# Kernel optimization log

Hardware: AMD Instinct MI355X
Metric: run time of the kernel (lower is better)

The kernel has to match this reference:

```python
import jax, jax.numpy as jnp
import numpy as np

N_WIN = 8
NUM_HEADS = 8
TOPK = 4
D_MODEL = 128
SCALE = D_MODEL ** (-0.5)


def setup_inputs() -> dict:
    key = jax.random.key(0)
    k1, k2 = jax.random.split(key)
    cv_feature = jax.random.normal(k1, (1, 128, 128, 128), dtype=jnp.float32)
    mv_feature = jax.random.normal(k2, (1, 2, 128, 128, 128), dtype=jnp.float32)
    return {"cv_feature": cv_feature, "mv_feature": mv_feature}


def reference(cv_feature, mv_feature):
    # cv_feature: [N, H, W, C] query view; mv_feature: [N, V, H, W, C] multi-view KV
    N, H, W, C = cv_feature.shape
    V = mv_feature.shape[1]
    j = i = N_WIN
    h, w = H // j, W // i
    p2, w2 = j * i, h * w
    ch = C // NUM_HEADS  # per-head dim

    # window partition: n (j h) (i w) c -> n (j i) h w c
    cv_patch = cv_feature.reshape(N, j, h, i, w, C).transpose(0, 1, 3, 2, 4, 5).reshape(N, p2, h, w, C)
    mv_patch = mv_feature.reshape(N, V, j, h, i, w, C).transpose(0, 1, 2, 4, 3, 5, 6).reshape(N, V, p2, h, w, C)

    q_pix = cv_patch.reshape(N, p2, w2, C)          # [N, p2, w2, C]
    kv_pix = mv_patch.reshape(N, V, p2, w2, C)      # [N, V, p2, w2, C]

    # window-level descriptors (means) -> routing logits
    q_win = cv_patch.mean(axis=(2, 3))              # [N, p2, C]
    k_win = mv_patch.mean(axis=(3, 4))              # [N, V, p2, C]

    # TopK routing (detached in original; forward math identical)
    k_flat = k_win.reshape(N, V * p2, C)
    attn_logit = jnp.einsum('npc,nqc->npq', q_win * SCALE, k_flat)  # [N, p2, V*p2]
    topk_logit, r_idx = jax.lax.top_k(attn_logit, TOPK)
    r_weight = jax.nn.softmax(topk_logit, axis=-1)  # computed by module, unused downstream

    # KV gather of selected windows: [N, p2, topk, w2, C]
    kv_flat = kv_pix.reshape(N, V * p2, w2, C)
    kv_sel = kv_flat[jnp.arange(N)[:, None, None], r_idx]

    # per-window multi-head attention over topk*w2 gathered tokens
    q = q_pix.reshape(N, p2, w2, NUM_HEADS, ch)
    kv = kv_sel.reshape(N, p2, TOPK * w2, NUM_HEADS, ch)
    attn = jnp.einsum('npwmc,npxmc->npmwx', q * SCALE, kv)  # [N, p2, m, w2, topk*w2]
    attn = jax.nn.softmax(attn, axis=-1)
    out = jnp.einsum('npmwx,npxmc->npwmc', attn, kv)        # [N, p2, w2, m, ch]

    # merge windows back: n (j i) (h w) c -> n (j h) (i w) c
    out = out.reshape(N, j, i, h, w, C).transpose(0, 1, 3, 2, 4, 5).reshape(N, H, W, C)
    return out
```

## Files before the change

### kernel.cpp

```cpp
#include <hip/hip_runtime.h>

#define HH_ 128
#define WW_ 128
#define CC_ 128
#define P2 64
#define W2 256
#define NH 8
#define CH 16
#define NV 2
#define TOPK 4
#define SCALE 0.08838834764831845f

typedef unsigned short u16;
typedef unsigned int   u32;
typedef short s8v __attribute__((ext_vector_type(8)));
typedef float f4  __attribute__((ext_vector_type(4)));

union FRAG { uint4 q; u32 u[4]; s8v v; };

__device__ float g_means[(P2 + NV * P2) * CC_];
__device__ int2  g_part[64];
__device__ int   g_mode;
__device__ int   g_amb;

__device__ inline u16 f2b(float v) {
    union { float f; u32 u; } x; x.f = v;
    u32 r = x.u + 0x7FFFu + ((x.u >> 16) & 1u);
    return (u16)(r >> 16);
}
__device__ inline float b2f(u16 h) {
    union { u32 u; float f; } x; x.u = (u32)h << 16; return x.f;
}
__device__ inline float h2f(u16 h) {
    u32 s = (h >> 15) & 1u, e = (h >> 10) & 31u, m = h & 1023u;
    float v;
    if (e == 0)       v = m * 5.9604644775e-8f;
    else if (e == 31) v = 65504.f;
    else { union { u32 u; float f; } x; x.u = ((e + 112u) << 23) | (m << 13); v = x.f; }
    return s ? -v : v;
}
__device__ inline u16 f2h(float v) {
    union { float f; u32 u; } x; x.f = v;
    u32 s = (x.u >> 16) & 0x8000u;
    int  e = (int)((x.u >> 23) & 0xFF) - 112;
    u32  m = x.u & 0x7FFFFF;
    if (e >= 31) return (u16)(s | 0x7BFF);
    if (e <= 0) {
        if (e < -10) return (u16)s;
        m |= 0x800000u;
        int sh = 14 - e;
        u32 r = m >> sh, rem = m & ((1u << sh) - 1u), half = 1u << (sh - 1);
        if (rem > half || (rem == half && (r & 1))) r++;
        return (u16)(s | r);
    }
    u32 r = ((u32)e << 10) | (m >> 13), rem = m & 0x1FFFu;
    if (rem > 0x1000u || (rem == 0x1000u && (r & 1))) r++;
    return (u16)(s | r);
}

__device__ inline u32 pkhi(float a, float b) {
    union { float f; u32 u; } xa, xb; xa.f = a; xb.f = b;
    return (xa.u >> 16) | (xb.u & 0xFFFF0000u);
}
__device__ inline float hipart(float a) {
    union { float f; u32 u; } x; x.f = a; x.u &= 0xFFFF0000u; return x.f;
}

template<int MODE>
__device__ inline float4 loadf4(const void* __restrict__ src, int off) {
    if (MODE == 0) return *(const float4*)((const float*)src + off);
    uint2 v = *(const uint2*)((const u16*)src + off);
    float4 r;
    if (MODE == 1) {
        r.x = b2f((u16)v.x); r.y = b2f((u16)(v.x >> 16));
        r.z = b2f((u16)v.y); r.w = b2f((u16)(v.y >> 16));
    } else {
        r.x = h2f((u16)v.x); r.y = h2f((u16)(v.x >> 16));
        r.z = h2f((u16)v.y); r.w = h2f((u16)(v.y >> 16));
    }
    return r;
}

template<int MODE>
__device__ inline void load16t(const void* __restrict__ src, int off, float* __restrict__ f) {
    if (MODE == 0) {
        const float4* p4 = (const float4*)((const float*)src + off);
#pragma unroll
        for (int i = 0; i < 4; ++i) {
            float4 v = p4[i];
            f[4 * i] = v.x; f[4 * i + 1] = v.y; f[4 * i + 2] = v.z; f[4 * i + 3] = v.w;
        }
    } else {
        const uint4* p4 = (const uint4*)((const u16*)src + off);
#pragma unroll
        for (int i = 0; i < 2; ++i) {
            uint4 v = p4[i];
            u32 wd[4] = { v.x, v.y, v.z, v.w };
#pragma unroll
            for (int j = 0; j < 4; ++j) {
                u16 lo = (u16)(wd[j] & 0xFFFFu), hi = (u16)(wd[j] >> 16);
                f[8 * i + 2 * j]     = (MODE == 1) ? b2f(lo) : h2f(lo);
                f[8 * i + 2 * j + 1] = (MODE == 1) ? b2f(hi) : h2f(hi);
            }
        }
    }
}

template<int MODE>
__device__ inline void store4t(void* __restrict__ out, int off, const float* __restrict__ r) {
    if (MODE == 0) {
        *(float4*)((float*)out + off) = make_float4(r[0], r[1], r[2], r[3]);
    } else if (MODE == 1) {
        u32 w0 = (u32)f2b(r[0]) | ((u32)f2b(r[1]) << 16);
        u32 w1 = (u32)f2b(r[2]) | ((u32)f2b(r[3]) << 16);
        *(uint2*)((u16*)out + off) = make_uint2(w0, w1);
    } else {
        u32 w0 = (u32)f2h(r[0]) | ((u32)f2h(r[1]) << 16);
        u32 w1 = (u32)f2h(r[2]) | ((u32)f2h(r[3]) << 16);
        *(uint2*)((u16*)out + off) = make_uint2(w0, w1);
    }
}

__global__ void detect_sample(const void* __restrict__ cv, int n) {
    __shared__ int bc[2];
    int tid = threadIdx.x, k = blockIdx.x;
    if (tid < 2) bc[tid] = 0;
    __syncthreads();
    int lim32 = n / 2;
    int lim16 = n / 2;
    u32 r = ((u32)(tid + k * 257) * 2654435761u);
    int j32 = (int)(r % (u32)lim32);
    float a = fabsf(((const float*)cv)[j32]);
    bool c0 = (a >= 1e-4f && a <= 1e4f);
    int j16 = 2 * (int)((r >> 8) % (u32)lim16);
    float b = fabsf(b2f(((const u16*)cv)[j16]));
    bool c1 = (b >= 1e-4f && b <= 1e4f);
    unsigned long long b0 = __ballot(c0);
    unsigned long long b1 = __ballot(c1);
    if ((tid & 63) == 0) {
        atomicAdd(&bc[0], __popcll(b0));
        atomicAdd(&bc[1], __popcll(b1));
    }
    __syncthreads();
    if (tid == 0) g_part[k] = make_int2(bc[0], bc[1]);
}

__global__ void detect_final() {
    int tid = threadIdx.x;
    int2 v = g_part[tid];
    int c0 = v.x, c1 = v.y;
#pragma unroll
    for (int off = 32; off >= 1; off >>= 1) {
        c0 += __shfl_down(c0, off);
        c1 += __shfl_down(c1, off);
    }
    if (tid == 0) {
        const float T = 256.f * 64.f;
        float f0 = c0 / T, f1 = c1 / T;
        int mode, amb = 0;
        if (f1 >= 0.85f) mode = 1;
        else if (f0 >= 0.80f) mode = 0;
        else mode = 2;
        if ((f1 > 0.60f && f1 < 0.85f) || (mode != 1 && f0 > 0.65f && f0 < 0.80f)) amb = 1;
        g_mode = mode; g_amb = amb;
    }
}

__global__ __launch_bounds__(512) void win_mean_kernel(const void* __restrict__ cv,
                                                       const void* __restrict__ mv) {
    __shared__ float sred[512];
    int mode = g_mode;
    int row = blockIdx.x;
    int tid = threadIdx.x;
    int c = tid & 127, q4 = tid >> 7;
    const void* src; size_t voff = 0; int p;
    if (row < P2) { p = row; src = cv; }
    else { int r = row - P2; voff = (size_t)(r >> 6) * HH_ * WW_ * CC_; p = r & 63; src = mv; }
    int jj = p >> 3, ii = p & 7;
    size_t base = voff + ((size_t)(jj * 16 + q4 * 4) * WW_ + ii * 16) * CC_ + c;
    float acc = 0.f;
    if (mode == 0) {
        const float* sp = (const float*)src;
        for (int hh = 0; hh < 4; ++hh) {
#pragma unroll
            for (int ww = 0; ww < 16; ++ww)
                acc += sp[base + ((size_t)hh * WW_ + ww) * CC_];
        }
    } else if (mode == 1) {
        const u16* sp = (const u16*)src;
        for (int hh = 0; hh < 4; ++hh) {
#pragma unroll
            for (int ww = 0; ww < 16; ++ww)
                acc += b2f(sp[base + ((size_t)hh * WW_ + ww) * CC_]);
        }
    } else {
        const u16* sp = (const u16*)src;
        for (int hh = 0; hh < 4; ++hh) {
#pragma unroll
            for (int ww = 0; ww < 16; ++ww)
                acc += h2f(sp[base + ((size_t)hh * WW_ + ww) * CC_]);
        }
    }
    sred[tid] = acc;
    __syncthreads();
    if (tid < 128) {
        float s = sred[tid] + sred[tid + 128] + sred[tid + 256] + sred[tid + 384];
        g_means[row * CC_ + tid] = s * (1.0f / 256.0f);
    }
}

template<int MODE>
__device__ void attn_body(const void* __restrict__ cv, const void* __restrict__ mv,
                          void* __restrict__ out, int p, int m, int tid,
                          u32 (* __restrict__ vfrag)[64][4], const int* __restrict__ rwin) {
    int jj = p >> 3, ii = p & 7;

#pragma unroll
    for (int it = 0; it < 2; ++it) {
        int kr = tid + it * 512;
        int kt = kr >> 4, r = kr & 15, g = r >> 2, iofs = r & 3;
        int t = rwin[kr >> 8];
        int v = t >> 6, pp = t & 63;
        int jj2 = pp >> 3, ii2 = pp & 7;
        int hh = (kr >> 4) & 15, ww = r;
        int kvbase = ((v * HH_ + jj2 * 16 + hh) * WW_ + ii2 * 16 + ww) * CC_ + m * CH;
        float f[CH];
        load16t<MODE>(mv, kvbase, f);
#pragma unroll
        for (int c = 0; c < CH; ++c) {
            union { float ff; u32 uu; } x; x.ff = f[c];
            u16 hi = (u16)(x.uu >> 16);
            union { float ff; u32 uu; } y; y.ff = f[c] - hipart(f[c]);
            u16 lo = (u16)(y.uu >> 16);
            u16* s = (u16*)&vfrag[kt][g * 16 + c][0];
            s[iofs] = hi; s[4 + iofs] = lo;
        }
    }

    int wv = tid >> 6, l = tid & 63;
    int lg = l >> 4, lr = l & 15;
    FRAG qf1[2], qf2[2];
#pragma unroll
    for (int qi = 0; qi < 2; ++qi) {
        int qrow = wv * 32 + qi * 16 + lr;
        int hh = qrow >> 4, ww = qrow & 15;
        int pix = (jj * 16 + hh) * WW_ + (ii * 16 + ww);
        float4 qv = loadf4<MODE>(cv, pix * CC_ + m * CH + 4 * lg);
        float q0 = qv.x * SCALE, q1 = qv.y * SCALE, q2 = qv.z * SCALE, q3 = qv.w * SCALE;
        u32 h01 = pkhi(q0, q1), h23 = pkhi(q2, q3);
        u32 l01 = pkhi(q0 - hipart(q0), q1 - hipart(q1));
        u32 l23 = pkhi(q2 - hipart(q2), q3 - hipart(q3));
        qf1[qi].u[0] = h01; qf1[qi].u[1] = h23; qf1[qi].u[2] = l01; qf1[qi].u[3] = l23;
        qf2[qi].u[0] = l01; qf2[qi].u[1] = l23; qf2[qi].u[2] = h01; qf2[qi].u[3] = h23;
    }

    int wb0, wb1, wb2, wb3;
#define MKWB(G, W) { int t = rwin[G]; int v = t >> 6, pp = t & 63;            \
        int jj2 = pp >> 3, ii2 = pp & 7;                                      \
        W = ((v * HH_ + jj2 * 16) * WW_ + ii2 * 16 + lr) * CC_ + m * CH + 4 * lg; }
    MKWB(0, wb0) MKWB(1, wb1) MKWB(2, wb2) MKWB(3, wb3)
#undef MKWB

    __syncthreads();

    float4 kA0 = loadf4<MODE>(mv, wb0);
    float4 kA1 = loadf4<MODE>(mv, wb0 + WW_ * CC_);
    f4 Oacc0 = {0.f, 0.f, 0.f, 0.f};
    f4 Oacc1 = {0.f, 0.f, 0.f, 0.f};
    float lp0 = 0.f, lp1 = 0.f;
    const u32* vbase = &vfrag[0][l][0];

#pragma unroll 2
    for (int kt = 0; kt < 64; ++kt) {
        float4 kc = (kt & 1) ? kA1 : kA0;
        {
            int ktn = kt + 2; ktn = (ktn > 63) ? 63 : ktn;
            int a = (ktn < 16) ? wb0 : (ktn < 32) ? wb1 : (ktn < 48) ? wb2 : wb3;
            a += (ktn & 15) * (WW_ * CC_);
            float4 nv = loadf4<MODE>(mv, a);
            if (kt & 1) kA1 = nv; else kA0 = nv;
        }
        FRAG kf;
        kf.u[0] = pkhi(kc.x, kc.y);
        kf.u[1] = pkhi(kc.z, kc.w);
        kf.u[2] = pkhi(kc.x - hipart(kc.x), kc.y - hipart(kc.y));
        kf.u[3] = pkhi(kc.z - hipart(kc.z), kc.w - hipart(kc.w));
        FRAG vf;
        vf.q = *(const uint4*)(vbase + kt * 256);

        {
            f4 sc = {0.f, 0.f, 0.f, 0.f};
            sc = __builtin_amdgcn_mfma_f32_16x16x32_bf16(kf.v, qf1[0].v, sc, 0, 0, 0);
            sc = __builtin_amdgcn_mfma_f32_16x16x32_bf16(kf.v, qf2[0].v, sc, 0, 0, 0);
            float pe0 = __expf(fminf(sc[0], 20.f));
            float pe1 = __expf(fminf(sc[1], 20.f));
            float pe2 = __expf(fminf(sc[2], 20.f));
            float pe3 = __expf(fminf(sc[3], 20.f));
            lp0 += (pe0 + pe1) + (pe2 + pe3);
            FRAG pf1, pf2;
            pf1.u[0] = pkhi(pe0, pe1);
            pf1.u[1] = pkhi(pe2, pe3);
            pf1.u[2] = pkhi(pe0 - hipart(pe0), pe1 - hipart(pe1));
            pf1.u[3] = pkhi(pe2 - hipart(pe2), pe3 - hipart(pe3));
            pf2.u[0] = pf1.u[2]; pf2.u[1] = pf1.u[3];
            pf2.u[2] = pf1.u[0]; pf2.u[3] = pf1.u[1];
            Oacc0 = __builtin_amdgcn_mfma_f32_16x16x32_bf16(vf.v, pf1.v, Oacc0, 0, 0, 0);
            Oacc0 = __builtin_amdgcn_mfma_f32_16x16x32_bf16(vf.v, pf2.v, Oacc0, 0, 0, 0);
        }
        {
            f4 sc = {0.f, 0.f, 0.f, 0.f};
            sc = __builtin_amdgcn_mfma_f32_16x16x32_bf16(kf.v, qf1[1].v, sc, 0, 0, 0);
            sc = __builtin_amdgcn_mfma_f32_16x16x32_bf16(kf.v, qf2[1].v, sc, 0, 0, 0);
            float pe0 = __expf(fminf(sc[0], 20.f));
            float pe1 = __expf(fminf(sc[1], 20.f));
            float pe2 = __expf(fminf(sc[2], 20.f));
            float pe3 = __expf(fminf(sc[3], 20.f));
            lp1 += (pe0 + pe1) + (pe2 + pe3);
            FRAG pf1, pf2;
            pf1.u[0] = pkhi(pe0, pe1);
            pf1.u[1] = pkhi(pe2, pe3);
            pf1.u[2] = pkhi(pe0 - hipart(pe0), pe1 - hipart(pe1));
            pf1.u[3] = pkhi(pe2 - hipart(pe2), pe3 - hipart(pe3));
            pf2.u[0] = pf1.u[2]; pf2.u[1] = pf1.u[3];
            pf2.u[2] = pf1.u[0]; pf2.u[3] = pf1.u[1];
            Oacc1 = __builtin_amdgcn_mfma_f32_16x16x32_bf16(vf.v, pf1.v, Oacc1, 0, 0, 0);
            Oacc1 = __builtin_amdgcn_mfma_f32_16x16x32_bf16(vf.v, pf2.v, Oacc1, 0, 0, 0);
        }
    }

#pragma unroll
    for (int qi = 0; qi < 2; ++qi) {
        float lt = (qi == 0) ? lp0 : lp1;
        lt += __shfl_xor(lt, 16);
        lt += __shfl_xor(lt, 32);
        float inv = 1.0f / fmaxf(lt, 1e-30f);
        f4 Oa = (qi == 0) ? Oacc0 : Oacc1;
        float res[4];
#pragma unroll
        for (int r = 0; r < 4; ++r)
            res[r] = fminf(fmaxf(Oa[r] * inv, -1000.f), 1000.f);
        int qrow = wv * 32 + qi * 16 + lr;
        int hh = qrow >> 4, ww = qrow & 15;
        int pix = (jj * 16 + hh) * WW_ + (ii * 16 + ww);
        store4t<MODE>(out, pix * CC_ + m * CH + 4 * lg, res);
    }
}

__global__ __launch_bounds__(512, 4) void attn_kernel(const void* __restrict__ cv,
                                                      const void* __restrict__ mv,
                                                      void* __restrict__ out) {
    __shared__ u32 vfrag[64][64][4];
    __shared__ float slog[NV * P2];
    __shared__ int   sridx[TOPK];

    int mode = g_mode;
    int p = blockIdx.x >> 3, m = blockIdx.x & 7;
    int tid = threadIdx.x;

    {
        int t  = tid >> 2;
        int cs = (tid & 3) << 5;
        const float4* qw = (const float4*)(g_means + p * CC_ + cs);
        const float4* kw = (const float4*)(g_means + (P2 + t) * CC_ + cs);
        float a = 0.f;
#pragma unroll
        for (int i = 0; i < 8; ++i) {
            float4 qv = qw[i], kv4 = kw[i];
            a += qv.x * kv4.x + qv.y * kv4.y + qv.z * kv4.z + qv.w * kv4.w;
        }
        a += __shfl_down(a, 2, 4);
        a += __shfl_down(a, 1, 4);
        if ((tid & 3) == 0) slog[t] = a;
    }
    __syncthreads();
    if (tid == 0) {
#pragma unroll
        for (int k = 0; k < TOPK; ++k) {
            int best = 0; float bv = slog[0];
            for (int q2 = 1; q2 < NV * P2; ++q2)
                if (slog[q2] > bv) { bv = slog[q2]; best = q2; }
            sridx[k] = best;
            slog[best] = -3.0e38f;
        }
    }
    __syncthreads();

    int rwin[TOPK];
#pragma unroll
    for (int k = 0; k < TOPK; ++k) rwin[k] = sridx[k] & 127;

    if (mode == 0)      attn_body<0>(cv, mv, out, p, m, tid, vfrag, rwin);
    else if (mode == 1) attn_body<1>(cv, mv, out, p, m, tid, vfrag, rwin);
    else                attn_body<2>(cv, mv, out, p, m, tid, vfrag, rwin);
}

extern "C" void kernel_launch(void* const* d_in, const int* in_sizes, int n_in,
                              void* d_out, int out_size, void* d_ws, size_t ws_size,
                              hipStream_t stream) {
    const void* cv = d_in[0];
    const void* mv = d_in[1];
    int n_cv = in_sizes[0];
    if (n_in >= 2 && in_sizes[0] > in_sizes[1]) { cv = d_in[1]; mv = d_in[0]; n_cv = in_sizes[1]; }
    (void)d_ws; (void)ws_size; (void)out_size;

    detect_sample<<<64, 256, 0, stream>>>(cv, n_cv);
    detect_final<<<1, 64, 0, stream>>>();
    win_mean_kernel<<<192, 512, 0, stream>>>(cv, mv);
    attn_kernel<<<P2 * NH, 512, 0, stream>>>(cv, mv, d_out);
}
```

Before: 150.5 us.

## Stage K and V fragments in shared memory in two halves with prefetch overlap

The attention kernel now pre-packs both K and V hi/lo bf16 fragments into shared memory. It does this in two 32-tile halves, loading the second half from global memory while computing the first. Previously only V was staged and K was converted per iteration from register prefetches. The window-mean kernel is also vectorized to 8-channel loads with a 32-way partial reduction. The cost is scalar strided V loads (decode1 per element), extra barriers and same-sized LDS use.

Result: faster. 142.1 us (-5.6%).

```diff
diff --git a/kernel.cpp b/kernel.cpp
--- a/kernel.cpp
+++ b/kernel.cpp
@@ -67,6 +67,13 @@
 }
 
 template<int MODE>
+__device__ inline float decode1(const void* __restrict__ src, int off) {
+    if (MODE == 0) return ((const float*)src)[off];
+    u16 h = ((const u16*)src)[off];
+    return (MODE == 1) ? b2f(h) : h2f(h);
+}
+
+template<int MODE>
 __device__ inline float4 loadf4(const void* __restrict__ src, int off) {
     if (MODE == 0) return *(const float4*)((const float*)src + off);
     uint2 v = *(const uint2*)((const u16*)src + off);
@@ -79,31 +86,6 @@
         r.z = h2f((u16)v.y); r.w = h2f((u16)(v.y >> 16));
     }
     return r;
-}
-
-template<int MODE>
-__device__ inline void load16t(const void* __restrict__ src, int off, float* __restrict__ f) {
-    if (MODE == 0) {
-        const float4* p4 = (const float4*)((const float*)src + off);
-#pragma unroll
-        for (int i = 0; i < 4; ++i) {
-            float4 v = p4[i];
-            f[4 * i] = v.x; f[4 * i + 1] = v.y; f[4 * i + 2] = v.z; f[4 * i + 3] = v.w;
-        }
-    } else {
-        const uint4* p4 = (const uint4*)((const u16*)src + off);
-#pragma unroll
-        for (int i = 0; i < 2; ++i) {
-            uint4 v = p4[i];
-            u32 wd[4] = { v.x, v.y, v.z, v.w };
-#pragma unroll
-            for (int j = 0; j < 4; ++j) {
-                u16 lo = (u16)(wd[j] & 0xFFFFu), hi = (u16)(wd[j] >> 16);
-                f[8 * i + 2 * j]     = (MODE == 1) ? b2f(lo) : h2f(lo);
-                f[8 * i + 2 * j + 1] = (MODE == 1) ? b2f(hi) : h2f(hi);
-            }
-        }
-    }
 }
 
 template<int MODE>
@@ -166,45 +148,56 @@
     }
 }
 
+template<int MODE>
+__device__ inline void wm_accum(const void* __restrict__ src, int voff, int jj, int ii,
+                                int pc, int c0, float* __restrict__ acc) {
+#pragma unroll
+    for (int k = 0; k < 8; ++k) {
+        int px = 8 * pc + k;
+        int hh = px >> 4, ww = px & 15;
+        int a = voff + ((jj * 16 + hh) * WW_ + ii * 16 + ww) * CC_ + c0;
+        if (MODE == 0) {
+            const float4* p4 = (const float4*)((const float*)src + a);
+            float4 x = p4[0], y = p4[1];
+            acc[0] += x.x; acc[1] += x.y; acc[2] += x.z; acc[3] += x.w;
+            acc[4] += y.x; acc[5] += y.y; acc[6] += y.z; acc[7] += y.w;
+        } else {
+            uint4 v = *(const uint4*)((const u16*)src + a);
+            u32 wd[4] = { v.x, v.y, v.z, v.w };
+#pragma unroll
+            for (int j = 0; j < 4; ++j) {
+                u16 lo = (u16)(wd[j] & 0xFFFFu), hi = (u16)(wd[j] >> 16);
+                acc[2 * j]     += (MODE == 1) ? b2f(lo) : h2f(lo);
+                acc[2 * j + 1] += (MODE == 1) ? b2f(hi) : h2f(hi);
+            }
+        }
+    }
+}
+
 __global__ __launch_bounds__(512) void win_mean_kernel(const void* __restrict__ cv,
                                                        const void* __restrict__ mv) {
-    __shared__ float sred[512];
+    __shared__ float part[32][128];
     int mode = g_mode;
-    int row = blockIdx.x;
-    int tid = threadIdx.x;
-    int c = tid & 127, q4 = tid >> 7;
-    const void* src; size_t voff = 0; int p;
+    int row = blockIdx.x, tid = threadIdx.x;
+    int o = tid & 15, pc = tid >> 4;
+    const void* src; int voff = 0; int p;
     if (row < P2) { p = row; src = cv; }
-    else { int r = row - P2; voff = (size_t)(r >> 6) * HH_ * WW_ * CC_; p = r & 63; src = mv; }
+    else { int r = row - P2; voff = (r >> 6) * HH_ * WW_ * CC_; p = r & 63; src = mv; }
     int jj = p >> 3, ii = p & 7;
-    size_t base = voff + ((size_t)(jj * 16 + q4 * 4) * WW_ + ii * 16) * CC_ + c;
-    float acc = 0.f;
-    if (mode == 0) {
-        const float* sp = (const float*)src;
-        for (int hh = 0; hh < 4; ++hh) {
-#pragma unroll
-            for (int ww = 0; ww < 16; ++ww)
-                acc += sp[base + ((size_t)hh * WW_ + ww) * CC_];
-        }
-    } else if (mode == 1) {
-        const u16* sp = (const u16*)src;
-        for (int hh = 0; hh < 4; ++hh) {
-#pragma unroll
-            for (int ww = 0; ww < 16; ++ww)
-                acc += b2f(sp[base + ((size_t)hh * WW_ + ww) * CC_]);
-        }
-    } else {
-        const u16* sp = (const u16*)src;
-        for (int hh = 0; hh < 4; ++hh) {
-#pragma unroll
-            for (int ww = 0; ww < 16; ++ww)
-                acc += h2f(sp[base + ((size_t)hh * WW_ + ww) * CC_]);
-        }
-    }
-    sred[tid] = acc;
+    int c0 = 8 * o;
+    float acc[8];
+#pragma unroll
+    for (int j = 0; j < 8; ++j) acc[j] = 0.f;
+    if (mode == 0)      wm_accum<0>(src, voff, jj, ii, pc, c0, acc);
+    else if (mode == 1) wm_accum<1>(src, voff, jj, ii, pc, c0, acc);
+    else                wm_accum<2>(src, voff, jj, ii, pc, c0, acc);
+#pragma unroll
+    for (int j = 0; j < 8; ++j) part[pc][c0 + j] = acc[j];
     __syncthreads();
     if (tid < 128) {
-        float s = sred[tid] + sred[tid + 128] + sred[tid + 256] + sred[tid + 384];
+        float s = 0.f;
+#pragma unroll
+        for (int k = 0; k < 32; ++k) s += part[k][tid];
         g_means[row * CC_ + tid] = s * (1.0f / 256.0f);
     }
 }
@@ -212,33 +205,13 @@
 template<int MODE>
 __device__ void attn_body(const void* __restrict__ cv, const void* __restrict__ mv,
                           void* __restrict__ out, int p, int m, int tid,
-                          u32 (* __restrict__ vfrag)[64][4], const int* __restrict__ rwin) {
+                          u32 (* __restrict__ kfrag)[64][4],
+                          u32 (* __restrict__ vfrag)[64][4],
+                          const int* __restrict__ rwin) {
     int jj = p >> 3, ii = p & 7;
-
-#pragma unroll
-    for (int it = 0; it < 2; ++it) {
-        int kr = tid + it * 512;
-        int kt = kr >> 4, r = kr & 15, g = r >> 2, iofs = r & 3;
-        int t = rwin[kr >> 8];
-        int v = t >> 6, pp = t & 63;
-        int jj2 = pp >> 3, ii2 = pp & 7;
-        int hh = (kr >> 4) & 15, ww = r;
-        int kvbase = ((v * HH_ + jj2 * 16 + hh) * WW_ + ii2 * 16 + ww) * CC_ + m * CH;
-        float f[CH];
-        load16t<MODE>(mv, kvbase, f);
-#pragma unroll
-        for (int c = 0; c < CH; ++c) {
-            union { float ff; u32 uu; } x; x.ff = f[c];
-            u16 hi = (u16)(x.uu >> 16);
-            union { float ff; u32 uu; } y; y.ff = f[c] - hipart(f[c]);
-            u16 lo = (u16)(y.uu >> 16);
-            u16* s = (u16*)&vfrag[kt][g * 16 + c][0];
-            s[iofs] = hi; s[4 + iofs] = lo;
-        }
-    }
-
     int wv = tid >> 6, l = tid & 63;
     int lg = l >> 4, lr = l & 15;
+
     FRAG qf1[2], qf2[2];
 #pragma unroll
     for (int qi = 0; qi < 2; ++qi) {
@@ -254,79 +227,119 @@
         qf2[qi].u[0] = l01; qf2[qi].u[1] = l23; qf2[qi].u[2] = h01; qf2[qi].u[3] = h23;
     }
 
-    int wb0, wb1, wb2, wb3;
-#define MKWB(G, W) { int t = rwin[G]; int v = t >> 6, pp = t & 63;            \
-        int jj2 = pp >> 3, ii2 = pp & 7;                                      \
-        W = ((v * HH_ + jj2 * 16) * WW_ + ii2 * 16 + lr) * CC_ + m * CH + 4 * lg; }
-    MKWB(0, wb0) MKWB(1, wb1) MKWB(2, wb2) MKWB(3, wb3)
-#undef MKWB
-
-    __syncthreads();
-
-    float4 kA0 = loadf4<MODE>(mv, wb0);
-    float4 kA1 = loadf4<MODE>(mv, wb0 + WW_ * CC_);
+    int ktl0 = tid >> 6;
+    int kb[4], vb[4];
+#pragma unroll
+    for (int g = 0; g < 4; ++g) {
+        int t = rwin[g]; int v = t >> 6, pp = t & 63;
+        int jj2 = pp >> 3, ii2 = pp & 7;
+        int wrow = (v * HH_ + jj2 * 16) * WW_ + ii2 * 16;
+        kb[g] = (wrow + lr) * CC_ + m * CH + 4 * lg;
+        vb[g] = (wrow + 4 * lg) * CC_ + m * CH + lr;
+    }
+
+    float4 kraw[4];
+    float  vraw[4][4];
+
+    auto loadh = [&](int h) {
+#pragma unroll
+        for (int i = 0; i < 4; ++i) {
+            int kt = h * 32 + ktl0 + 8 * i;
+            int g = kt >> 4, hh2 = kt & 15;
+            kraw[i] = loadf4<MODE>(mv, kb[g] + hh2 * (WW_ * CC_));
+        }
+#pragma unroll
+        for (int i = 0; i < 4; ++i) {
+            int kt = h * 32 + ktl0 + 8 * i;
+            int g = kt >> 4, hh2 = kt & 15;
+            int a = vb[g] + hh2 * (WW_ * CC_);
+#pragma unroll
+            for (int io = 0; io < 4; ++io)
+                vraw[i][io] = decode1<MODE>(mv, a + io * CC_);
+        }
+    };
+
+    auto writeh = [&]() {
+#pragma unroll
+        for (int i = 0; i < 4; ++i) {
+            int ktl = ktl0 + 8 * i;
+            float4 kc = kraw[i];
+            FRAG kf;
+            kf.u[0] = pkhi(kc.x, kc.y);
+            kf.u[1] = pkhi(kc.z, kc.w);
+            kf.u[2] = pkhi(kc.x - hipart(kc.x), kc.y - hipart(kc.y));
+            kf.u[3] = pkhi(kc.z - hipart(kc.z), kc.w - hipart(kc.w));
+            *(uint4*)&kfrag[ktl][l][0] = kf.q;
+            float v0 = vraw[i][0], v1 = vraw[i][1], v2 = vraw[i][2], v3 = vraw[i][3];
+            FRAG vf;
+            vf.u[0] = pkhi(v0, v1);
+            vf.u[1] = pkhi(v2, v3);
+            vf.u[2] = pkhi(v0 - hipart(v0), v1 - hipart(v1));
+            vf.u[3] = pkhi(v2 - hipart(v2), v3 - hipart(v3));
+            *(uint4*)&vfrag[ktl][l][0] = vf.q;
+        }
+    };
+
     f4 Oacc0 = {0.f, 0.f, 0.f, 0.f};
     f4 Oacc1 = {0.f, 0.f, 0.f, 0.f};
     float lp0 = 0.f, lp1 = 0.f;
-    const u32* vbase = &vfrag[0][l][0];
-
+    const uint4* kbase = (const uint4*)&kfrag[0][0][0];
+    const uint4* vbase = (const uint4*)&vfrag[0][0][0];
+
+    auto computeh = [&]() {
 #pragma unroll 2
-    for (int kt = 0; kt < 64; ++kt) {
-        float4 kc = (kt & 1) ? kA1 : kA0;
-        {
-            int ktn = kt + 2; ktn = (ktn > 63) ? 63 : ktn;
-            int a = (ktn < 16) ? wb0 : (ktn < 32) ? wb1 : (ktn < 48) ? wb2 : wb3;
-            a += (ktn & 15) * (WW_ * CC_);
-            float4 nv = loadf4<MODE>(mv, a);
-            if (kt & 1) kA1 = nv; else kA0 = nv;
-        }
-        FRAG kf;
-        kf.u[0] = pkhi(kc.x, kc.y);
-        kf.u[1] = pkhi(kc.z, kc.w);
-        kf.u[2] = pkhi(kc.x - hipart(kc.x), kc.y - hipart(kc.y));
-        kf.u[3] = pkhi(kc.z - hipart(kc.z), kc.w - hipart(kc.w));
-        FRAG vf;
-        vf.q = *(const uint4*)(vbase + kt * 256);
-
-        {
-            f4 sc = {0.f, 0.f, 0.f, 0.f};
-            sc = __builtin_amdgcn_mfma_f32_16x16x32_bf16(kf.v, qf1[0].v, sc, 0, 0, 0);
-            sc = __builtin_amdgcn_mfma_f32_16x16x32_bf16(kf.v, qf2[0].v, sc, 0, 0, 0);
-            float pe0 = __expf(fminf(sc[0], 20.f));
-            float pe1 = __expf(fminf(sc[1], 20.f));
-            float pe2 = __expf(fminf(sc[2], 20.f));
-            float pe3 = __expf(fminf(sc[3], 20.f));
-            lp0 += (pe0 + pe1) + (pe2 + pe3);
-            FRAG pf1, pf2;
-            pf1.u[0] = pkhi(pe0, pe1);
-            pf1.u[1] = pkhi(pe2, pe3);
-            pf1.u[2] = pkhi(pe0 - hipart(pe0), pe1 - hipart(pe1));
-            pf1.u[3] = pkhi(pe2 - hipart(pe2), pe3 - hipart(pe3));
-            pf2.u[0] = pf1.u[2]; pf2.u[1] = pf1.u[3];
-            pf2.u[2] = pf1.u[0]; pf2.u[3] = pf1.u[1];
-            Oacc0 = __builtin_amdgcn_mfma_f32_16x16x32_bf16(vf.v, pf1.v, Oacc0, 0, 0, 0);
-            Oacc0 = __builtin_amdgcn_mfma_f32_16x16x32_bf16(vf.v, pf2.v, Oacc0, 0, 0, 0);
-        }
-        {
-            f4 sc = {0.f, 0.f, 0.f, 0.f};
-            sc = __builtin_amdgcn_mfma_f32_16x16x32_bf16(kf.v, qf1[1].v, sc, 0, 0, 0);
-            sc = __builtin_amdgcn_mfma_f32_16x16x32_bf16(kf.v, qf2[1].v, sc, 0, 0, 0);
-            float pe0 = __expf(fminf(sc[0], 20.f));
-            float pe1 = __expf(fminf(sc[1], 20.f));
-            float pe2 = __expf(fminf(sc[2], 20.f));
-            float pe3 = __expf(fminf(sc[3], 20.f));
-            lp1 += (pe0 + pe1) + (pe2 + pe3);
-            FRAG pf1, pf2;
-            pf1.u[0] = pkhi(pe0, pe1);
-            pf1.u[1] = pkhi(pe2, pe3);
-            pf1.u[2] = pkhi(pe0 - hipart(pe0), pe1 - hipart(pe1));
-            pf1.u[3] = pkhi(pe2 - hipart(pe2), pe3 - hipart(pe3));
-            pf2.u[0] = pf1.u[2]; pf2.u[1] = pf1.u[3];
-            pf2.u[2] = pf1.u[0]; pf2.u[3] = pf1.u[1];
-            Oacc1 = __builtin_amdgcn_mfma_f32_16x16x32_bf16(vf.v, pf1.v, Oacc1, 0, 0, 0);
-            Oacc1 = __builtin_amdgcn_mfma_f32_16x16x32_bf16(vf.v, pf2.v, Oacc1, 0, 0, 0);
-        }
-    }
+        for (int ktl = 0; ktl < 32; ++ktl) {
+            FRAG kf, vf, vf2;
+            kf.q = kbase[ktl * 64 + l];
+            vf.q = vbase[ktl * 64 + l];
+            vf2.u[0] = vf.u[2]; vf2.u[1] = vf.u[3];
+            vf2.u[2] = vf.u[0]; vf2.u[3] = vf.u[1];
+            {
+                f4 sc = {0.f, 0.f, 0.f, 0.f};
+                sc = __builtin_amdgcn_mfma_f32_16x16x32_bf16(kf.v, qf1[0].v, sc, 0, 0, 0);
+                sc = __builtin_amdgcn_mfma_f32_16x16x32_bf16(kf.v, qf2[0].v, sc, 0, 0, 0);
+                float pe0 = __expf(fminf(sc[0], 20.f));
+                float pe1 = __expf(fminf(sc[1], 20.f));
+                float pe2 = __expf(fminf(sc[2], 20.f));
+                float pe3 = __expf(fminf(sc[3], 20.f));
+                lp0 += (pe0 + pe1) + (pe2 + pe3);
+                FRAG pf;
+                pf.u[0] = pkhi(pe0, pe1);
+                pf.u[1] = pkhi(pe2, pe3);
+                pf.u[2] = pkhi(pe0 - hipart(pe0), pe1 - hipart(pe1));
+                pf.u[3] = pkhi(pe2 - hipart(pe2), pe3 - hipart(pe3));
+                Oacc0 = __builtin_amdgcn_mfma_f32_16x16x32_bf16(vf.v,  pf.v, Oacc0, 0, 0, 0);
+                Oacc0 = __builtin_amdgcn_mfma_f32_16x16x32_bf16(vf2.v, pf.v, Oacc0, 0, 0, 0);
+            }
+            {
+                f4 sc = {0.f, 0.f, 0.f, 0.f};
+                sc = __builtin_amdgcn_mfma_f32_16x16x32_bf16(kf.v, qf1[1].v, sc, 0, 0, 0);
+                sc = __builtin_amdgcn_mfma_f32_16x16x32_bf16(kf.v, qf2[1].v, sc, 0, 0, 0);
+                float pe0 = __expf(fminf(sc[0], 20.f));
+                float pe1 = __expf(fminf(sc[1], 20.f));
+                float pe2 = __expf(fminf(sc[2], 20.f));
+                float pe3 = __expf(fminf(sc[3], 20.f));
+                lp1 += (pe0 + pe1) + (pe2 + pe3);
+                FRAG pf;
+                pf.u[0] = pkhi(pe0, pe1);
+                pf.u[1] = pkhi(pe2, pe3);
+                pf.u[2] = pkhi(pe0 - hipart(pe0), pe1 - hipart(pe1));
+                pf.u[3] = pkhi(pe2 - hipart(pe2), pe3 - hipart(pe3));
+                Oacc1 = __builtin_amdgcn_mfma_f32_16x16x32_bf16(vf.v,  pf.v, Oacc1, 0, 0, 0);
+                Oacc1 = __builtin_amdgcn_mfma_f32_16x16x32_bf16(vf2.v, pf.v, Oacc1, 0, 0, 0);
+            }
+        }
+    };
+
+    loadh(0);
+    writeh();
+    __syncthreads();
+    loadh(1);
+    computeh();
+    __syncthreads();
+    writeh();
+    __syncthreads();
+    computeh();
 
 #pragma unroll
     for (int qi = 0; qi < 2; ++qi) {
@@ -349,7 +362,8 @@
 __global__ __launch_bounds__(512, 4) void attn_kernel(const void* __restrict__ cv,
                                                       const void* __restrict__ mv,
                                                       void* __restrict__ out) {
-    __shared__ u32 vfrag[64][64][4];
+    __shared__ u32 kfrag[32][64][4];
+    __shared__ u32 vfrag[32][64][4];
     __shared__ float slog[NV * P2];
     __shared__ int   sridx[TOPK];
 
@@ -389,9 +403,9 @@
 #pragma unroll
     for (int k = 0; k < TOPK; ++k) rwin[k] = sridx[k] & 127;
 
-    if (mode == 0)      attn_body<0>(cv, mv, out, p, m, tid, vfrag, rwin);
-    else if (mode == 1) attn_body<1>(cv, mv, out, p, m, tid, vfrag, rwin);
-    else                attn_body<2>(cv, mv, out, p, m, tid, vfrag, rwin);
+    if (mode == 0)      attn_body<0>(cv, mv, out, p, m, tid, kfrag, vfrag, rwin);
+    else if (mode == 1) attn_body<1>(cv, mv, out, p, m, tid, kfrag, vfrag, rwin);
+    else                attn_body<2>(cv, mv, out, p, m, tid, kfrag, vfrag, rwin);
 }
 
 extern "C" void kernel_launch(void* const* d_in, const int* in_sizes, int n_in,
```
